# Kernel optimization log

Hardware: AMD Instinct MI355X
Metric: run time of the kernel (lower is better)

Reference implementation:

```python
import jax, jax.numpy as jnp
import numpy as np

N_NODES = 50000
N_EDGES = 800000
FEAT = 128
HID = 64
N_CLS = 12


def setup_inputs() -> dict:
    key = jax.random.key(0)
    ks = jax.random.split(key, 8)
    x = jax.random.normal(ks[0], (N_NODES, FEAT), dtype=jnp.float32)
    edge_index = jax.random.randint(ks[1], (2, N_EDGES), 0, N_NODES, dtype=jnp.int64)
    s1 = 1.0 / np.sqrt(FEAT)
    s2 = 1.0 / np.sqrt(HID)
    W1 = jax.random.uniform(ks[2], (FEAT, HID), jnp.float32, -s1, s1)
    b1 = jnp.zeros((HID,), jnp.float32)
    W2 = jax.random.uniform(ks[3], (HID, HID), jnp.float32, -s2, s2)
    b2 = jnp.zeros((HID,), jnp.float32)
    Wfc = jax.random.uniform(ks[4], (HID, N_CLS), jnp.float32, -s2, s2)
    bfc = jax.random.uniform(ks[5], (N_CLS,), jnp.float32, -s2, s2)
    return {"x": x, "edge_index": edge_index, "W1": W1, "b1": b1,
            "W2": W2, "b2": b2, "Wfc": Wfc, "bfc": bfc}


def gcn_conv(x, W, b, src, dst, n_nodes):
    """PyG GCNConv: symmetric-normalized aggregation with self-loops.
    out_i = sum_{j in N(i)} (xW)_j / sqrt(d_i d_j) + (xW)_i / d_i + b,
    where d = in-degree + 1 (self loop)."""
    xw = x @ W  # [N, out] -- transform before propagate (PyG order)
    deg = jnp.zeros((n_nodes,), x.dtype).at[dst].add(1.0) + 1.0
    dinv = jax.lax.rsqrt(deg)
    norm = dinv[src] * dinv[dst]  # [E]
    agg = jax.ops.segment_sum(xw[src] * norm[:, None], dst, num_segments=n_nodes)
    agg = agg + xw * (dinv * dinv)[:, None]  # self-loop term
    return agg + b


def reference(x, edge_index, W1, b1, W2, b2, Wfc, bfc):
    n = x.shape[0]
    src, dst = edge_index[0], edge_index[1]
    h = jax.nn.relu(gcn_conv(x, W1, b1, src, dst, n))
    h = jax.nn.relu(gcn_conv(h, W2, b2, src, dst, n))
    return h @ Wfc + bfc  # [N, num_content_categories]
```

## Files before the change

kernel.cpp:

```cpp
#include <hip/hip_runtime.h>
#include <hip/hip_fp16.h>


#define CAP   64
#define NBUK  196
#define ET    4096
#define BCAP  5120

typedef unsigned short u16;
typedef unsigned long long u64;
typedef _Float16 f16;
typedef _Float16 f16x8 __attribute__((ext_vector_type(8)));
typedef float f32x4 __attribute__((ext_vector_type(4)));

__global__ __launch_bounds__(256) void k_prep(const float* __restrict__ W1,
                                              const float* __restrict__ W2,
                                              f16* __restrict__ W1t,
                                              f16* __restrict__ W2t,
                                              int* __restrict__ gcur) {
    int i = blockIdx.x * 256 + threadIdx.x;
    if (i < NBUK) gcur[i] = 0;
    if (i < 128 * 64) {
        int k = i >> 6, nn = i & 63;
        W1t[nn * 128 + k] = (f16)W1[k * 64 + nn];
    }
    int j = i - 128 * 64;
    if (j >= 0 && j < 64 * 64) {
        int k = j >> 6, nn = j & 63;
        W2t[nn * 64 + k] = (f16)W2[k * 64 + nn];
    }
}

__global__ __launch_bounds__(256) void k_scat(const int* __restrict__ src,
                                              const int* __restrict__ dst,
                                              int* __restrict__ gcur,
                                              unsigned* __restrict__ eb, int E) {
    __shared__ int hist[NBUK];
    __shared__ int cur[NBUK];
    const int tid = threadIdx.x, blk = blockIdx.x;
    for (int i = tid; i < NBUK; i += 256) hist[i] = 0;
    __syncthreads();

    const int e0 = blk * ET;
    unsigned pk[16];
    if (e0 + ET <= E) {
        const int4* s4 = (const int4*)(src + e0);
        const int4* d4 = (const int4*)(dst + e0);
#pragma unroll
        for (int j = 0; j < ET / 1024; j++) {
            int4 sv = s4[j * 256 + tid];
            int4 dv = d4[j * 256 + tid];
            pk[4 * j + 0] = ((unsigned)dv.x << 16) | (unsigned)sv.x;
            pk[4 * j + 1] = ((unsigned)dv.y << 16) | (unsigned)sv.y;
            pk[4 * j + 2] = ((unsigned)dv.z << 16) | (unsigned)sv.z;
            pk[4 * j + 3] = ((unsigned)dv.w << 16) | (unsigned)sv.w;
            atomicAdd(&hist[(unsigned)dv.x >> 8], 1);
            atomicAdd(&hist[(unsigned)dv.y >> 8], 1);
            atomicAdd(&hist[(unsigned)dv.z >> 8], 1);
            atomicAdd(&hist[(unsigned)dv.w >> 8], 1);
        }
    } else {
#pragma unroll
        for (int j = 0; j < ET / 256; j++) {
            int e = e0 + j * 256 + tid;
            unsigned u = 0xffffffffu;
            if (e < E) {
                unsigned d = (unsigned)dst[e];
                u = (d << 16) | (unsigned)src[e];
                atomicAdd(&hist[d >> 8], 1);
            }
            pk[j] = u;
        }
    }
    __syncthreads();
    for (int b = tid; b < NBUK; b += 256)
        cur[b] = b * BCAP + atomicAdd(&gcur[b], hist[b]);
    __syncthreads();
#pragma unroll
    for (int j = 0; j < 16; j++) {
        unsigned u = pk[j];
        if (u != 0xffffffffu) eb[atomicAdd(&cur[u >> 24], 1)] = u;
    }
}

__global__ __launch_bounds__(1024) void k_buildb(const unsigned* __restrict__ eb,
                                                 const int* __restrict__ gcur,
                                                 u16* __restrict__ csr,
                                                 int* __restrict__ cnt, int n) {
    __shared__ u16 lcsr[256 * CAP];
    __shared__ int cur[256];
    const int tid = threadIdx.x, b = blockIdx.x;
    if (tid < 256) cur[tid] = 0;
    __syncthreads();
    const int e0 = b * BCAP, e1 = e0 + gcur[b];
    for (int e = e0 + tid; e < e1; e += 1024) {
        unsigned u = __builtin_nontemporal_load(eb + e);
        int ld = (int)((u >> 16) & 255u);
        int p = atomicAdd(&cur[ld], 1);
        if (p < CAP) lcsr[ld * CAP + p] = (u16)(u & 0xffffu);
    }
    __syncthreads();
    const int node0 = b * 256;
    for (int i = tid; i < 256 * CAP / 8; i += 1024) {
        int r = i / (CAP / 8), q = i % (CAP / 8);
        int c = cur[r] < CAP ? cur[r] : CAP;
        uint4 v = *(uint4*)&lcsr[r * CAP + q * 8];
        if (q * 8 >= c) v = make_uint4(0, 0, 0, 0);
        *(uint4*)&csr[(size_t)(node0 + r) * CAP + q * 8] = v;
    }
    if (tid < 256 && node0 + tid < n) cnt[node0 + tid] = cur[tid];
}

template <int K, bool IS_HALF, typename TIN>
__global__ __launch_bounds__(256) void k_gemm(const TIN* __restrict__ X,
                                              const f16* __restrict__ Wt,
                                              const int* __restrict__ cnt,
                                              __half* __restrict__ Y, int n) {
    constexpr int KS = K + 8;
    __shared__ f16 xsh[64 * KS];
    __shared__ f16 wsh[64 * KS];
    const int tid = threadIdx.x;
    const int row0 = blockIdx.x * 64;

    for (int i = tid; i < 64 * (K / 8); i += 256) {
        int nn = i / (K / 8), kq = i % (K / 8);
        *(uint4*)&wsh[nn * KS + 8 * kq] = *(const uint4*)&Wt[nn * K + 8 * kq];
    }
    if constexpr (IS_HALF) {
        const __half* Xh = (const __half*)X;
        for (int i = tid; i < 64 * (K / 8); i += 256) {
            int r = i / (K / 8), kq = i % (K / 8);
            uint4 u = make_uint4(0, 0, 0, 0);
            int row = row0 + r;
            if (row < n) u = *(const uint4*)&Xh[(size_t)row * K + 8 * kq];
            *(uint4*)&xsh[r * KS + 8 * kq] = u;
        }
    } else {
        const float* Xf = (const float*)X;
        for (int i = tid; i < 64 * (K / 4); i += 256) {
            int r = i / (K / 4), q4 = i % (K / 4);
            float4 v = make_float4(0.f, 0.f, 0.f, 0.f);
            int row = row0 + r;
            if (row < n) v = *(const float4*)&Xf[(size_t)row * K + 4 * q4];
            __half2 p0 = __floats2half2_rn(v.x, v.y);
            __half2 p1 = __floats2half2_rn(v.z, v.w);
            uint2 o = make_uint2(*(unsigned*)&p0, *(unsigned*)&p1);
            *(uint2*)&xsh[r * KS + 4 * q4] = o;
        }
    }
    __syncthreads();

    const int wv = tid >> 6;
    const int lane = tid & 63;
    const int mn = lane & 15;
    const int q = lane >> 4;

    f32x4 acc[4] = {{0, 0, 0, 0}, {0, 0, 0, 0}, {0, 0, 0, 0}, {0, 0, 0, 0}};
    const f16* arow = &xsh[(16 * wv + mn) * KS + 8 * q];
#pragma unroll
    for (int s = 0; s < K / 32; s++) {
        f16x8 A = *(const f16x8*)&arow[32 * s];
#pragma unroll
        for (int c = 0; c < 4; c++) {
            f16x8 B = *(const f16x8*)&wsh[(16 * c + mn) * KS + 32 * s + 8 * q];
            acc[c] = __builtin_amdgcn_mfma_f32_16x16x32_f16(A, B, acc[c], 0, 0, 0);
        }
    }

    const int rowb = row0 + 16 * wv + 4 * q;
    float dinv[4];
#pragma unroll
    for (int r = 0; r < 4; r++)
        dinv[r] = rsqrtf((float)((rowb + r < n) ? cnt[rowb + r] : 0) + 1.0f);
#pragma unroll
    for (int c = 0; c < 4; c++)
#pragma unroll
        for (int r = 0; r < 4; r++) {
            int row = rowb + r;
            if (row < n)
                Y[(size_t)row * 64 + 16 * c + mn] = __float2half(acc[c][r] * dinv[r]);
        }
}

__device__ __forceinline__ float4 gather_node(const __half* __restrict__ y,
                                              const u16* __restrict__ lst,
                                              int deg, int c4) {
    float4 a0 = make_float4(0.f, 0.f, 0.f, 0.f);
    float4 a1 = make_float4(0.f, 0.f, 0.f, 0.f);
    int i = 0;
    for (; i + 16 <= deg; i += 16) {
        const u64* lp = (const u64*)(lst + i);
        u64 q0 = __builtin_nontemporal_load(lp);
        u64 q1 = __builtin_nontemporal_load(lp + 1);
        u64 q2 = __builtin_nontemporal_load(lp + 2);
        u64 q3 = __builtin_nontemporal_load(lp + 3);
        unsigned idx[16];
#pragma unroll
        for (int t = 0; t < 4; t++) {
            idx[t]      = (unsigned)((q0 >> (16 * t)) & 0xffffu);
            idx[t + 4]  = (unsigned)((q1 >> (16 * t)) & 0xffffu);
            idx[t + 8]  = (unsigned)((q2 >> (16 * t)) & 0xffffu);
            idx[t + 12] = (unsigned)((q3 >> (16 * t)) & 0xffffu);
        }
        uint2 v[16];
#pragma unroll
        for (int t = 0; t < 16; t++) v[t] = *(const uint2*)&y[(size_t)idx[t] * 64 + 4 * c4];
#pragma unroll
        for (int t = 0; t < 16; t += 2) {
            float2 lo0 = __half22float2(*(__half2*)&v[t].x);
            float2 hi0 = __half22float2(*(__half2*)&v[t].y);
            float2 lo1 = __half22float2(*(__half2*)&v[t + 1].x);
            float2 hi1 = __half22float2(*(__half2*)&v[t + 1].y);
            a0.x += lo0.x; a0.y += lo0.y; a0.z += hi0.x; a0.w += hi0.y;
            a1.x += lo1.x; a1.y += lo1.y; a1.z += hi1.x; a1.w += hi1.y;
        }
    }
    if (i + 8 <= deg) {
        const u64* lp = (const u64*)(lst + i);
        u64 q0 = __builtin_nontemporal_load(lp);
        u64 q1 = __builtin_nontemporal_load(lp + 1);
        unsigned idx[8];
#pragma unroll
        for (int t = 0; t < 4; t++) {
            idx[t]     = (unsigned)((q0 >> (16 * t)) & 0xffffu);
            idx[t + 4] = (unsigned)((q1 >> (16 * t)) & 0xffffu);
        }
        uint2 v[8];
#pragma unroll
        for (int t = 0; t < 8; t++) v[t] = *(const uint2*)&y[(size_t)idx[t] * 64 + 4 * c4];
#pragma unroll
        for (int t = 0; t < 8; t += 2) {
            float2 lo0 = __half22float2(*(__half2*)&v[t].x);
            float2 hi0 = __half22float2(*(__half2*)&v[t].y);
            float2 lo1 = __half22float2(*(__half2*)&v[t + 1].x);
            float2 hi1 = __half22float2(*(__half2*)&v[t + 1].y);
            a0.x += lo0.x; a0.y += lo0.y; a0.z += hi0.x; a0.w += hi0.y;
            a1.x += lo1.x; a1.y += lo1.y; a1.z += hi1.x; a1.w += hi1.y;
        }
        i += 8;
    }
    if (i + 4 <= deg) {
        u64 q0 = __builtin_nontemporal_load((const u64*)(lst + i));
        unsigned idx[4];
#pragma unroll
        for (int t = 0; t < 4; t++) idx[t] = (unsigned)((q0 >> (16 * t)) & 0xffffu);
        uint2 v[4];
#pragma unroll
        for (int t = 0; t < 4; t++) v[t] = *(const uint2*)&y[(size_t)idx[t] * 64 + 4 * c4];
#pragma unroll
        for (int t = 0; t < 4; t += 2) {
            float2 lo0 = __half22float2(*(__half2*)&v[t].x);
            float2 hi0 = __half22float2(*(__half2*)&v[t].y);
            float2 lo1 = __half22float2(*(__half2*)&v[t + 1].x);
            float2 hi1 = __half22float2(*(__half2*)&v[t + 1].y);
            a0.x += lo0.x; a0.y += lo0.y; a0.z += hi0.x; a0.w += hi0.y;
            a1.x += lo1.x; a1.y += lo1.y; a1.z += hi1.x; a1.w += hi1.y;
        }
        i += 4;
    }
    for (; i < deg; i++) {
        uint2 vv = *(const uint2*)&y[(size_t)lst[i] * 64 + 4 * c4];
        float2 lo = __half22float2(*(__half2*)&vv.x);
        float2 hi = __half22float2(*(__half2*)&vv.y);
        a0.x += lo.x; a0.y += lo.y; a0.z += hi.x; a0.w += hi.y;
    }
    return make_float4(a0.x + a1.x, a0.y + a1.y, a0.z + a1.z, a0.w + a1.w);
}

__global__ __launch_bounds__(256) void k_agg1g2(const __half* __restrict__ y,
                                                const u16* __restrict__ csr,
                                                const int* __restrict__ cnt,
                                                const float* __restrict__ bias,
                                                const f16* __restrict__ W2t,
                                                __half* __restrict__ y2, int n) {
    constexpr int KS2 = 64 + 8;
    __shared__ f16 ash[16 * KS2];
    __shared__ f16 wsh[64 * KS2];
    __shared__ float dsh[16];
    const int tid = threadIdx.x;
    const int node0 = blockIdx.x * 16;

    for (int i = tid; i < 64 * 8; i += 256) {
        int nn = i >> 3, kq = i & 7;
        *(uint4*)&wsh[nn * KS2 + 8 * kq] = *(const uint4*)&W2t[nn * 64 + 8 * kq];
    }

    const int c4 = tid & 15;
    const int r16 = tid >> 4;
    const int node = node0 + r16;
    const int nodeC = node < n ? node : 0;
    int deg_raw = (node < n) ? cnt[node] : 0;
    int deg = deg_raw > CAP ? CAP : deg_raw;
    float4 acc = gather_node(y, csr + (size_t)nodeC * CAP, deg, c4);
    uint2 sv = *(const uint2*)&y[(size_t)nodeC * 64 + 4 * c4];
    float2 slo = __half22float2(*(__half2*)&sv.x);
    float2 shi = __half22float2(*(__half2*)&sv.y);
    float d = rsqrtf((float)deg_raw + 1.0f);
    float4 bv = *(const float4*)&bias[4 * c4];
    float v0 = fmaxf(fmaf(d, acc.x + slo.x, bv.x), 0.f);
    float v1 = fmaxf(fmaf(d, acc.y + slo.y, bv.y), 0.f);
    float v2 = fmaxf(fmaf(d, acc.z + shi.x, bv.z), 0.f);
    float v3 = fmaxf(fmaf(d, acc.w + shi.y, bv.w), 0.f);
    __half2 o0 = __floats2half2_rn(v0, v1);
    __half2 o1 = __floats2half2_rn(v2, v3);
    u64 packed = (u64)(*(unsigned*)&o0) | ((u64)(*(unsigned*)&o1) << 32);
    *(u64*)&ash[r16 * KS2 + 4 * c4] = packed;
    if (c4 == 0) dsh[r16] = d;
    __syncthreads();

    const int wv = tid >> 6;
    const int lane = tid & 63;
    const int mn = lane & 15;
    const int q = lane >> 4;
    f32x4 acc2 = {0, 0, 0, 0};
#pragma unroll
    for (int s = 0; s < 2; s++) {
        f16x8 A = *(const f16x8*)&ash[mn * KS2 + 32 * s + 8 * q];
        f16x8 B = *(const f16x8*)&wsh[(16 * wv + mn) * KS2 + 32 * s + 8 * q];
        acc2 = __builtin_amdgcn_mfma_f32_16x16x32_f16(A, B, acc2, 0, 0, 0);
    }
#pragma unroll
    for (int r = 0; r < 4; r++) {
        int row = node0 + 4 * q + r;
        if (row < n)
            y2[(size_t)row * 64 + 16 * wv + mn] =
                __float2half(acc2[r] * dsh[4 * q + r]);
    }
}

__global__ __launch_bounds__(256) void k_agg2fc(const __half* __restrict__ y,
                                                const u16* __restrict__ csr,
                                                const int* __restrict__ cnt,
                                                const float* __restrict__ bias,
                                                const float* __restrict__ Wfc,
                                                const float* __restrict__ bfc,
                                                float* __restrict__ out, int n) {
    __shared__ float wf[12 * 64];
    __shared__ float bf[12];
    const int tid = threadIdx.x;
    for (int i = tid; i < 12 * 64; i += 256) {
        int c = i >> 6, k = i & 63;
        wf[i] = Wfc[k * 12 + c];
    }
    if (tid < 12) bf[tid] = bfc[tid];
    __syncthreads();

    const int c4 = tid & 15;
    const int node = blockIdx.x * 16 + (tid >> 4);
    if (node >= n) return;
    int deg_raw = cnt[node];
    int deg = deg_raw > CAP ? CAP : deg_raw;
    float4 acc = gather_node(y, csr + node * CAP, deg, c4);
    uint2 sv = *(const uint2*)&y[(size_t)node * 64 + 4 * c4];
    float2 slo = __half22float2(*(__half2*)&sv.x);
    float2 shi = __half22float2(*(__half2*)&sv.y);
    float d = rsqrtf((float)deg_raw + 1.0f);
    float4 bv = *(const float4*)&bias[4 * c4];
    float v0 = fmaxf(fmaf(d, acc.x + slo.x, bv.x), 0.f);
    float v1 = fmaxf(fmaf(d, acc.y + slo.y, bv.y), 0.f);
    float v2 = fmaxf(fmaf(d, acc.z + shi.x, bv.z), 0.f);
    float v3 = fmaxf(fmaf(d, acc.w + shi.y, bv.w), 0.f);

    float res = 0.f;
#pragma unroll
    for (int c = 0; c < 12; c++) {
        float4 wv = *(const float4*)&wf[c * 64 + 4 * c4];
        float p = v0 * wv.x + v1 * wv.y + v2 * wv.z + v3 * wv.w;
        p += __shfl_xor(p, 1);
        p += __shfl_xor(p, 2);
        p += __shfl_xor(p, 4);
        p += __shfl_xor(p, 8);
        if (c4 == c) res = p + bf[c];
    }
    if (c4 < 12) out[(size_t)node * 12 + c4] = res;
}

extern "C" void kernel_launch(void* const* d_in, const int* in_sizes, int n_in,
                              void* d_out, int out_size, void* d_ws, size_t ws_size,
                              hipStream_t stream) {
    const float* x   = (const float*)d_in[0];
    const int*   ei  = (const int*)d_in[1];
    const float* W1  = (const float*)d_in[2];
    const float* b1  = (const float*)d_in[3];
    const float* W2  = (const float*)d_in[4];
    const float* b2  = (const float*)d_in[5];
    const float* Wfc = (const float*)d_in[6];
    const float* bfc = (const float*)d_in[7];
    float* out = (float*)d_out;

    const int n = in_sizes[0] / 128;
    const int E = in_sizes[1] / 2;
    const int* src = ei;
    const int* dst = ei + E;
    const int nblk = (E + ET - 1) / ET;

    char* w = (char*)d_ws;
    unsigned* eb  = (unsigned*)w;  w += (size_t)NBUK * BCAP * 4;
    int* gcur     = (int*)w;       w += 256 * 4;
    int* cnt      = (int*)w;       w += (size_t)((n + 63) / 64) * 64 * 4;
    f16* W1t      = (f16*)w;       w += 128 * 64 * 2;
    f16* W2t      = (f16*)w;       w += 64 * 64 * 2 + 256;
    u16* csr      = (u16*)w;       w += (size_t)NBUK * 256 * CAP * 2;
    __half* y     = (__half*)w;    w += (size_t)n * 64 * 2;
    __half* y2    = (__half*)w;

    k_prep   <<<dim3(48), dim3(256), 0, stream>>>(W1, W2, W1t, W2t, gcur);
    k_scat   <<<dim3(nblk), dim3(256), 0, stream>>>(src, dst, gcur, eb, E);
    k_buildb <<<dim3(NBUK), dim3(1024), 0, stream>>>(eb, gcur, csr, cnt, n);
    k_gemm<128, false, float><<<dim3((n + 63) / 64), dim3(256), 0, stream>>>(x, W1t, cnt, y, n);
    k_agg1g2 <<<dim3((n + 15) / 16), dim3(256), 0, stream>>>(y, csr, cnt, b1, W2t, y2, n);
    k_agg2fc <<<dim3((n + 15) / 16), dim3(256), 0, stream>>>(y2, csr, cnt, b2, Wfc, bfc, out, n);
}
```

Before: 156.7 us.

## Split neighbor lists by source half and gather in two passes per persistent block

The CSR build now keeps each node's neighbours in two 32-slot halves, split by whether the source index is below n/2, and packs both counts into one int. The aggregation kernels become persistent blocks (grid 1024) that first gather the low-half neighbours for all their node groups into shared memory, then gather the high-half and finish. Each pass then touches only half of the feature table, which is meant to improve L2/cache locality of the random gathers. The cost is more passes, a lower per-half cap (degree over 32 in one half gets truncated), extra shared memory, and a fixed NG_MAX=4 that assumes ngroups ≤ 4096.

Result: slower. 188.5 us (+20.3%).

```diff
diff --git a/kernel.cpp b/kernel.cpp
--- a/kernel.cpp
+++ b/kernel.cpp
@@ -3,9 +3,12 @@
 
 
 #define CAP   64
+#define HCAP  32
 #define NBUK  196
 #define ET    4096
 #define BCAP  5120
+#define AGG_GRID 1024
+#define NG_MAX 4
 
 typedef unsigned short u16;
 typedef unsigned long long u64;
@@ -86,37 +89,42 @@
 __global__ __launch_bounds__(1024) void k_buildb(const unsigned* __restrict__ eb,
                                                  const int* __restrict__ gcur,
                                                  u16* __restrict__ csr,
-                                                 int* __restrict__ cnt, int n) {
+                                                 int* __restrict__ cnt,
+                                                 int n, int hthr) {
     __shared__ u16 lcsr[256 * CAP];
-    __shared__ int cur[256];
+    __shared__ int cur[512];
     const int tid = threadIdx.x, b = blockIdx.x;
-    if (tid < 256) cur[tid] = 0;
+    if (tid < 512) cur[tid] = 0;
     __syncthreads();
     const int e0 = b * BCAP, e1 = e0 + gcur[b];
     for (int e = e0 + tid; e < e1; e += 1024) {
         unsigned u = __builtin_nontemporal_load(eb + e);
         int ld = (int)((u >> 16) & 255u);
-        int p = atomicAdd(&cur[ld], 1);
-        if (p < CAP) lcsr[ld * CAP + p] = (u16)(u & 0xffffu);
+        int srcv = (int)(u & 0xffffu);
+        int hf = srcv >= hthr;
+        int p = atomicAdd(&cur[ld * 2 + hf], 1);
+        if (p < HCAP) lcsr[ld * CAP + hf * HCAP + p] = (u16)srcv;
     }
     __syncthreads();
     const int node0 = b * 256;
     for (int i = tid; i < 256 * CAP / 8; i += 1024) {
-        int r = i / (CAP / 8), q = i % (CAP / 8);
-        int c = cur[r] < CAP ? cur[r] : CAP;
+        int r = i >> 3, q = i & 7;
+        int hf = q >= (HCAP / 8);
+        int cc = cur[r * 2 + hf]; if (cc > HCAP) cc = HCAP;
+        int off = q * 8 - hf * HCAP;
         uint4 v = *(uint4*)&lcsr[r * CAP + q * 8];
-        if (q * 8 >= c) v = make_uint4(0, 0, 0, 0);
+        if (off >= cc) v = make_uint4(0, 0, 0, 0);
         *(uint4*)&csr[(size_t)(node0 + r) * CAP + q * 8] = v;
     }
-    if (tid < 256 && node0 + tid < n) cnt[node0 + tid] = cur[tid];
-}
-
-template <int K, bool IS_HALF, typename TIN>
-__global__ __launch_bounds__(256) void k_gemm(const TIN* __restrict__ X,
-                                              const f16* __restrict__ Wt,
-                                              const int* __restrict__ cnt,
-                                              __half* __restrict__ Y, int n) {
-    constexpr int KS = K + 8;
+    if (tid < 256 && node0 + tid < n)
+        cnt[node0 + tid] = cur[tid * 2] | (cur[tid * 2 + 1] << 16);
+}
+
+__global__ __launch_bounds__(256) void k_gemm1(const float* __restrict__ X,
+                                               const f16* __restrict__ Wt,
+                                               const int* __restrict__ cnt,
+                                               __half* __restrict__ Y, int n) {
+    constexpr int K = 128, KS = K + 8;
     __shared__ f16 xsh[64 * KS];
     __shared__ f16 wsh[64 * KS];
     const int tid = threadIdx.x;
@@ -126,27 +134,15 @@
         int nn = i / (K / 8), kq = i % (K / 8);
         *(uint4*)&wsh[nn * KS + 8 * kq] = *(const uint4*)&Wt[nn * K + 8 * kq];
     }
-    if constexpr (IS_HALF) {
-        const __half* Xh = (const __half*)X;
-        for (int i = tid; i < 64 * (K / 8); i += 256) {
-            int r = i / (K / 8), kq = i % (K / 8);
-            uint4 u = make_uint4(0, 0, 0, 0);
-            int row = row0 + r;
-            if (row < n) u = *(const uint4*)&Xh[(size_t)row * K + 8 * kq];
-            *(uint4*)&xsh[r * KS + 8 * kq] = u;
-        }
-    } else {
-        const float* Xf = (const float*)X;
-        for (int i = tid; i < 64 * (K / 4); i += 256) {
-            int r = i / (K / 4), q4 = i % (K / 4);
-            float4 v = make_float4(0.f, 0.f, 0.f, 0.f);
-            int row = row0 + r;
-            if (row < n) v = *(const float4*)&Xf[(size_t)row * K + 4 * q4];
-            __half2 p0 = __floats2half2_rn(v.x, v.y);
-            __half2 p1 = __floats2half2_rn(v.z, v.w);
-            uint2 o = make_uint2(*(unsigned*)&p0, *(unsigned*)&p1);
-            *(uint2*)&xsh[r * KS + 4 * q4] = o;
-        }
+    for (int i = tid; i < 64 * (K / 4); i += 256) {
+        int r = i / (K / 4), q4 = i % (K / 4);
+        float4 v = make_float4(0.f, 0.f, 0.f, 0.f);
+        int row = row0 + r;
+        if (row < n) v = *(const float4*)&X[(size_t)row * K + 4 * q4];
+        __half2 p0 = __floats2half2_rn(v.x, v.y);
+        __half2 p1 = __floats2half2_rn(v.z, v.w);
+        uint2 o = make_uint2(*(unsigned*)&p0, *(unsigned*)&p1);
+        *(uint2*)&xsh[r * KS + 4 * q4] = o;
     }
     __syncthreads();
 
@@ -170,8 +166,10 @@
     const int rowb = row0 + 16 * wv + 4 * q;
     float dinv[4];
 #pragma unroll
-    for (int r = 0; r < 4; r++)
-        dinv[r] = rsqrtf((float)((rowb + r < n) ? cnt[rowb + r] : 0) + 1.0f);
+    for (int r = 0; r < 4; r++) {
+        int cp = (rowb + r < n) ? cnt[rowb + r] : 0;
+        dinv[r] = rsqrtf((float)((cp & 0xffff) + (cp >> 16)) + 1.0f);
+    }
 #pragma unroll
     for (int c = 0; c < 4; c++)
 #pragma unroll
@@ -267,18 +265,20 @@
     return make_float4(a0.x + a1.x, a0.y + a1.y, a0.z + a1.z, a0.w + a1.w);
 }
 
-__global__ __launch_bounds__(256) void k_agg1g2(const __half* __restrict__ y,
-                                                const u16* __restrict__ csr,
-                                                const int* __restrict__ cnt,
-                                                const float* __restrict__ bias,
-                                                const f16* __restrict__ W2t,
-                                                __half* __restrict__ y2, int n) {
+__global__ __launch_bounds__(256, 4) void k_agg1g2(const __half* __restrict__ y,
+                                                   const u16* __restrict__ csr,
+                                                   const int* __restrict__ cnt,
+                                                   const float* __restrict__ bias,
+                                                   const f16* __restrict__ W2t,
+                                                   __half* __restrict__ y2, int n) {
     constexpr int KS2 = 64 + 8;
     __shared__ f16 ash[16 * KS2];
     __shared__ f16 wsh[64 * KS2];
     __shared__ float dsh[16];
+    __shared__ float4 pash[NG_MAX][256];
     const int tid = threadIdx.x;
-    const int node0 = blockIdx.x * 16;
+    const int G = gridDim.x;
+    const int ngroups = (n + 15) >> 4;
 
     for (int i = tid; i < 64 * 8; i += 256) {
         int nn = i >> 3, kq = i & 7;
@@ -287,57 +287,78 @@
 
     const int c4 = tid & 15;
     const int r16 = tid >> 4;
-    const int node = node0 + r16;
-    const int nodeC = node < n ? node : 0;
-    int deg_raw = (node < n) ? cnt[node] : 0;
-    int deg = deg_raw > CAP ? CAP : deg_raw;
-    float4 acc = gather_node(y, csr + (size_t)nodeC * CAP, deg, c4);
-    uint2 sv = *(const uint2*)&y[(size_t)nodeC * 64 + 4 * c4];
-    float2 slo = __half22float2(*(__half2*)&sv.x);
-    float2 shi = __half22float2(*(__half2*)&sv.y);
-    float d = rsqrtf((float)deg_raw + 1.0f);
-    float4 bv = *(const float4*)&bias[4 * c4];
-    float v0 = fmaxf(fmaf(d, acc.x + slo.x, bv.x), 0.f);
-    float v1 = fmaxf(fmaf(d, acc.y + slo.y, bv.y), 0.f);
-    float v2 = fmaxf(fmaf(d, acc.z + shi.x, bv.z), 0.f);
-    float v3 = fmaxf(fmaf(d, acc.w + shi.y, bv.w), 0.f);
-    __half2 o0 = __floats2half2_rn(v0, v1);
-    __half2 o1 = __floats2half2_rn(v2, v3);
-    u64 packed = (u64)(*(unsigned*)&o0) | ((u64)(*(unsigned*)&o1) << 32);
-    *(u64*)&ash[r16 * KS2 + 4 * c4] = packed;
-    if (c4 == 0) dsh[r16] = d;
-    __syncthreads();
-
-    const int wv = tid >> 6;
-    const int lane = tid & 63;
-    const int mn = lane & 15;
-    const int q = lane >> 4;
-    f32x4 acc2 = {0, 0, 0, 0};
-#pragma unroll
-    for (int s = 0; s < 2; s++) {
-        f16x8 A = *(const f16x8*)&ash[mn * KS2 + 32 * s + 8 * q];
-        f16x8 B = *(const f16x8*)&wsh[(16 * wv + mn) * KS2 + 32 * s + 8 * q];
-        acc2 = __builtin_amdgcn_mfma_f32_16x16x32_f16(A, B, acc2, 0, 0, 0);
-    }
-#pragma unroll
-    for (int r = 0; r < 4; r++) {
-        int row = node0 + 4 * q + r;
-        if (row < n)
-            y2[(size_t)row * 64 + 16 * wv + mn] =
-                __float2half(acc2[r] * dsh[4 * q + r]);
-    }
-}
-
-__global__ __launch_bounds__(256) void k_agg2fc(const __half* __restrict__ y,
-                                                const u16* __restrict__ csr,
-                                                const int* __restrict__ cnt,
-                                                const float* __restrict__ bias,
-                                                const float* __restrict__ Wfc,
-                                                const float* __restrict__ bfc,
-                                                float* __restrict__ out, int n) {
+
+    int gi = 0;
+    for (int g = blockIdx.x; g < ngroups; g += G, ++gi) {
+        const int node = g * 16 + r16;
+        const int nodeC = node < n ? node : 0;
+        int cp = (node < n) ? cnt[node] : 0;
+        int dlo = cp & 0xffff; if (dlo > HCAP) dlo = HCAP;
+        pash[gi][tid] = gather_node(y, csr + (size_t)nodeC * CAP, dlo, c4);
+    }
+
+    gi = 0;
+    for (int g = blockIdx.x; g < ngroups; g += G, ++gi) {
+        const int node0g = g * 16;
+        const int node = node0g + r16;
+        const int nodeC = node < n ? node : 0;
+        int cp = (node < n) ? cnt[node] : 0;
+        int dlo_raw = cp & 0xffff, dhi_raw = cp >> 16;
+        int dhi = dhi_raw > HCAP ? HCAP : dhi_raw;
+        float4 acc = gather_node(y, csr + (size_t)nodeC * CAP + HCAP, dhi, c4);
+        float4 pa = pash[gi][tid];
+        acc.x += pa.x; acc.y += pa.y; acc.z += pa.z; acc.w += pa.w;
+        uint2 sv = *(const uint2*)&y[(size_t)nodeC * 64 + 4 * c4];
+        float2 slo = __half22float2(*(__half2*)&sv.x);
+        float2 shi = __half22float2(*(__half2*)&sv.y);
+        float d = rsqrtf((float)(dlo_raw + dhi_raw) + 1.0f);
+        float4 bv = *(const float4*)&bias[4 * c4];
+        float v0 = fmaxf(fmaf(d, acc.x + slo.x, bv.x), 0.f);
+        float v1 = fmaxf(fmaf(d, acc.y + slo.y, bv.y), 0.f);
+        float v2 = fmaxf(fmaf(d, acc.z + shi.x, bv.z), 0.f);
+        float v3 = fmaxf(fmaf(d, acc.w + shi.y, bv.w), 0.f);
+        __half2 o0 = __floats2half2_rn(v0, v1);
+        __half2 o1 = __floats2half2_rn(v2, v3);
+        u64 packed = (u64)(*(unsigned*)&o0) | ((u64)(*(unsigned*)&o1) << 32);
+        *(u64*)&ash[r16 * KS2 + 4 * c4] = packed;
+        if (c4 == 0) dsh[r16] = d;
+        __syncthreads();
+
+        const int wv = tid >> 6;
+        const int lane = tid & 63;
+        const int mn = lane & 15;
+        const int q = lane >> 4;
+        f32x4 acc2 = {0, 0, 0, 0};
+#pragma unroll
+        for (int s = 0; s < 2; s++) {
+            f16x8 A = *(const f16x8*)&ash[mn * KS2 + 32 * s + 8 * q];
+            f16x8 B = *(const f16x8*)&wsh[(16 * wv + mn) * KS2 + 32 * s + 8 * q];
+            acc2 = __builtin_amdgcn_mfma_f32_16x16x32_f16(A, B, acc2, 0, 0, 0);
+        }
+#pragma unroll
+        for (int r = 0; r < 4; r++) {
+            int row = node0g + 4 * q + r;
+            if (row < n)
+                y2[(size_t)row * 64 + 16 * wv + mn] =
+                    __float2half(acc2[r] * dsh[4 * q + r]);
+        }
+        __syncthreads();
+    }
+}
+
+__global__ __launch_bounds__(256, 4) void k_agg2fc(const __half* __restrict__ y,
+                                                   const u16* __restrict__ csr,
+                                                   const int* __restrict__ cnt,
+                                                   const float* __restrict__ bias,
+                                                   const float* __restrict__ Wfc,
+                                                   const float* __restrict__ bfc,
+                                                   float* __restrict__ out, int n) {
     __shared__ float wf[12 * 64];
     __shared__ float bf[12];
+    __shared__ float4 pash[NG_MAX][256];
     const int tid = threadIdx.x;
+    const int G = gridDim.x;
+    const int ngroups = (n + 15) >> 4;
     for (int i = tid; i < 12 * 64; i += 256) {
         int c = i >> 6, k = i & 63;
         wf[i] = Wfc[k * 12 + c];
@@ -346,33 +367,50 @@
     __syncthreads();
 
     const int c4 = tid & 15;
-    const int node = blockIdx.x * 16 + (tid >> 4);
-    if (node >= n) return;
-    int deg_raw = cnt[node];
-    int deg = deg_raw > CAP ? CAP : deg_raw;
-    float4 acc = gather_node(y, csr + node * CAP, deg, c4);
-    uint2 sv = *(const uint2*)&y[(size_t)node * 64 + 4 * c4];
-    float2 slo = __half22float2(*(__half2*)&sv.x);
-    float2 shi = __half22float2(*(__half2*)&sv.y);
-    float d = rsqrtf((float)deg_raw + 1.0f);
-    float4 bv = *(const float4*)&bias[4 * c4];
-    float v0 = fmaxf(fmaf(d, acc.x + slo.x, bv.x), 0.f);
-    float v1 = fmaxf(fmaf(d, acc.y + slo.y, bv.y), 0.f);
-    float v2 = fmaxf(fmaf(d, acc.z + shi.x, bv.z), 0.f);
-    float v3 = fmaxf(fmaf(d, acc.w + shi.y, bv.w), 0.f);
-
-    float res = 0.f;
-#pragma unroll
-    for (int c = 0; c < 12; c++) {
-        float4 wv = *(const float4*)&wf[c * 64 + 4 * c4];
-        float p = v0 * wv.x + v1 * wv.y + v2 * wv.z + v3 * wv.w;
-        p += __shfl_xor(p, 1);
-        p += __shfl_xor(p, 2);
-        p += __shfl_xor(p, 4);
-        p += __shfl_xor(p, 8);
-        if (c4 == c) res = p + bf[c];
-    }
-    if (c4 < 12) out[(size_t)node * 12 + c4] = res;
+    const int r16 = tid >> 4;
+
+    int gi = 0;
+    for (int g = blockIdx.x; g < ngroups; g += G, ++gi) {
+        const int node = g * 16 + r16;
+        const int nodeC = node < n ? node : 0;
+        int cp = (node < n) ? cnt[node] : 0;
+        int dlo = cp & 0xffff; if (dlo > HCAP) dlo = HCAP;
+        pash[gi][tid] = gather_node(y, csr + (size_t)nodeC * CAP, dlo, c4);
+    }
+
+    gi = 0;
+    for (int g = blockIdx.x; g < ngroups; g += G, ++gi) {
+        const int node = g * 16 + r16;
+        const int nodeC = node < n ? node : 0;
+        int cp = (node < n) ? cnt[node] : 0;
+        int dlo_raw = cp & 0xffff, dhi_raw = cp >> 16;
+        int dhi = dhi_raw > HCAP ? HCAP : dhi_raw;
+        float4 acc = gather_node(y, csr + (size_t)nodeC * CAP + HCAP, dhi, c4);
+        float4 pa = pash[gi][tid];
+        acc.x += pa.x; acc.y += pa.y; acc.z += pa.z; acc.w += pa.w;
+        uint2 sv = *(const uint2*)&y[(size_t)nodeC * 64 + 4 * c4];
+        float2 slo = __half22float2(*(__half2*)&sv.x);
+        float2 shi = __half22float2(*(__half2*)&sv.y);
+        float d = rsqrtf((float)(dlo_raw + dhi_raw) + 1.0f);
+        float4 bv = *(const float4*)&bias[4 * c4];
+        float v0 = fmaxf(fmaf(d, acc.x + slo.x, bv.x), 0.f);
+        float v1 = fmaxf(fmaf(d, acc.y + slo.y, bv.y), 0.f);
+        float v2 = fmaxf(fmaf(d, acc.z + shi.x, bv.z), 0.f);
+        float v3 = fmaxf(fmaf(d, acc.w + shi.y, bv.w), 0.f);
+
+        float res = 0.f;
+#pragma unroll
+        for (int c = 0; c < 12; c++) {
+            float4 wv = *(const float4*)&wf[c * 64 + 4 * c4];
+            float p = v0 * wv.x + v1 * wv.y + v2 * wv.z + v3 * wv.w;
+            p += __shfl_xor(p, 1);
+            p += __shfl_xor(p, 2);
+            p += __shfl_xor(p, 4);
+            p += __shfl_xor(p, 8);
+            if (c4 == c) res = p + bf[c];
+        }
+        if (c4 < 12 && node < n) out[(size_t)node * 12 + c4] = res;
+    }
 }
 
 extern "C" void kernel_launch(void* const* d_in, const int* in_sizes, int n_in,
@@ -406,8 +444,8 @@
 
     k_prep   <<<dim3(48), dim3(256), 0, stream>>>(W1, W2, W1t, W2t, gcur);
     k_scat   <<<dim3(nblk), dim3(256), 0, stream>>>(src, dst, gcur, eb, E);
-    k_buildb <<<dim3(NBUK), dim3(1024), 0, stream>>>(eb, gcur, csr, cnt, n);
-    k_gemm<128, false, float><<<dim3((n + 63) / 64), dim3(256), 0, stream>>>(x, W1t, cnt, y, n);
-    k_agg1g2 <<<dim3((n + 15) / 16), dim3(256), 0, stream>>>(y, csr, cnt, b1, W2t, y2, n);
-    k_agg2fc <<<dim3((n + 15) / 16), dim3(256), 0, stream>>>(y2, csr, cnt, b2, Wfc, bfc, out, n);
-}
+    k_buildb <<<dim3(NBUK), dim3(1024), 0, stream>>>(eb, gcur, csr, cnt, n, n / 2);
+    k_gemm1  <<<dim3((n + 63) / 64), dim3(256), 0, stream>>>(x, W1t, cnt, y, n);
+    k_agg1g2 <<<dim3(AGG_GRID), dim3(256), 0, stream>>>(y, csr, cnt, b1, W2t, y2, n);
+    k_agg2fc <<<dim3(AGG_GRID), dim3(256), 0, stream>>>(y2, csr, cnt, b2, Wfc, bfc, out, n);
+}
```

## Merge edge scatter and first GEMM into one launch, defer degree scaling

Applied to the files above, without the earlier changes.

The edge bucketing kernel and the layer-1 X*W1 GEMM now run as disjoint block ranges of a single launch, so the GEMM no longer waits for the degree count. The GEMM writes an unscaled fp32 intermediate, and the CSR build kernel then applies the rsqrt degree scaling and converts to fp16. This removes one kernel launch and its dependency bubble. In exchange it adds an extra fp32 write and read of an N x 64 buffer and more LDS per block in the merged kernel, which may reduce occupancy for the scatter blocks.

Result: no change. 156.4 us (-0.2%).

```diff
diff --git a/kernel.cpp b/kernel.cpp
--- a/kernel.cpp
+++ b/kernel.cpp
@@ -31,62 +31,119 @@
     }
 }
 
-__global__ __launch_bounds__(256) void k_scat(const int* __restrict__ src,
-                                              const int* __restrict__ dst,
-                                              int* __restrict__ gcur,
-                                              unsigned* __restrict__ eb, int E) {
+__global__ __launch_bounds__(256) void k_scatgemm(const int* __restrict__ src,
+                                                  const int* __restrict__ dst,
+                                                  int* __restrict__ gcur,
+                                                  unsigned* __restrict__ eb, int E,
+                                                  const float* __restrict__ X,
+                                                  const f16* __restrict__ W1t,
+                                                  float* __restrict__ Z,
+                                                  int n, int nblk) {
+    constexpr int K = 128, KS = K + 8;
+    __shared__ f16 xsh[64 * KS];
+    __shared__ f16 wsh[64 * KS];
     __shared__ int hist[NBUK];
     __shared__ int cur[NBUK];
-    const int tid = threadIdx.x, blk = blockIdx.x;
-    for (int i = tid; i < NBUK; i += 256) hist[i] = 0;
-    __syncthreads();
-
-    const int e0 = blk * ET;
-    unsigned pk[16];
-    if (e0 + ET <= E) {
-        const int4* s4 = (const int4*)(src + e0);
-        const int4* d4 = (const int4*)(dst + e0);
-#pragma unroll
-        for (int j = 0; j < ET / 1024; j++) {
-            int4 sv = s4[j * 256 + tid];
-            int4 dv = d4[j * 256 + tid];
-            pk[4 * j + 0] = ((unsigned)dv.x << 16) | (unsigned)sv.x;
-            pk[4 * j + 1] = ((unsigned)dv.y << 16) | (unsigned)sv.y;
-            pk[4 * j + 2] = ((unsigned)dv.z << 16) | (unsigned)sv.z;
-            pk[4 * j + 3] = ((unsigned)dv.w << 16) | (unsigned)sv.w;
-            atomicAdd(&hist[(unsigned)dv.x >> 8], 1);
-            atomicAdd(&hist[(unsigned)dv.y >> 8], 1);
-            atomicAdd(&hist[(unsigned)dv.z >> 8], 1);
-            atomicAdd(&hist[(unsigned)dv.w >> 8], 1);
+    const int tid = threadIdx.x;
+
+    if (blockIdx.x < (unsigned)nblk) {
+        const int blk = blockIdx.x;
+        for (int i = tid; i < NBUK; i += 256) hist[i] = 0;
+        __syncthreads();
+
+        const int e0 = blk * ET;
+        unsigned pk[16];
+        if (e0 + ET <= E) {
+            const int4* s4 = (const int4*)(src + e0);
+            const int4* d4 = (const int4*)(dst + e0);
+#pragma unroll
+            for (int j = 0; j < ET / 1024; j++) {
+                int4 sv = s4[j * 256 + tid];
+                int4 dv = d4[j * 256 + tid];
+                pk[4 * j + 0] = ((unsigned)dv.x << 16) | (unsigned)sv.x;
+                pk[4 * j + 1] = ((unsigned)dv.y << 16) | (unsigned)sv.y;
+                pk[4 * j + 2] = ((unsigned)dv.z << 16) | (unsigned)sv.z;
+                pk[4 * j + 3] = ((unsigned)dv.w << 16) | (unsigned)sv.w;
+                atomicAdd(&hist[(unsigned)dv.x >> 8], 1);
+                atomicAdd(&hist[(unsigned)dv.y >> 8], 1);
+                atomicAdd(&hist[(unsigned)dv.z >> 8], 1);
+                atomicAdd(&hist[(unsigned)dv.w >> 8], 1);
+            }
+        } else {
+#pragma unroll
+            for (int j = 0; j < ET / 256; j++) {
+                int e = e0 + j * 256 + tid;
+                unsigned u = 0xffffffffu;
+                if (e < E) {
+                    unsigned d = (unsigned)dst[e];
+                    u = (d << 16) | (unsigned)src[e];
+                    atomicAdd(&hist[d >> 8], 1);
+                }
+                pk[j] = u;
+            }
+        }
+        __syncthreads();
+        for (int b = tid; b < NBUK; b += 256)
+            cur[b] = b * BCAP + atomicAdd(&gcur[b], hist[b]);
+        __syncthreads();
+#pragma unroll
+        for (int j = 0; j < 16; j++) {
+            unsigned u = pk[j];
+            if (u != 0xffffffffu) eb[atomicAdd(&cur[u >> 24], 1)] = u;
         }
     } else {
-#pragma unroll
-        for (int j = 0; j < ET / 256; j++) {
-            int e = e0 + j * 256 + tid;
-            unsigned u = 0xffffffffu;
-            if (e < E) {
-                unsigned d = (unsigned)dst[e];
-                u = (d << 16) | (unsigned)src[e];
-                atomicAdd(&hist[d >> 8], 1);
+        const int row0 = (blockIdx.x - nblk) * 64;
+
+        for (int i = tid; i < 64 * (K / 8); i += 256) {
+            int nn = i / (K / 8), kq = i % (K / 8);
+            *(uint4*)&wsh[nn * KS + 8 * kq] = *(const uint4*)&W1t[nn * K + 8 * kq];
+        }
+        for (int i = tid; i < 64 * (K / 4); i += 256) {
+            int r = i / (K / 4), q4 = i % (K / 4);
+            float4 v = make_float4(0.f, 0.f, 0.f, 0.f);
+            int row = row0 + r;
+            if (row < n) v = *(const float4*)&X[(size_t)row * K + 4 * q4];
+            __half2 p0 = __floats2half2_rn(v.x, v.y);
+            __half2 p1 = __floats2half2_rn(v.z, v.w);
+            uint2 o = make_uint2(*(unsigned*)&p0, *(unsigned*)&p1);
+            *(uint2*)&xsh[r * KS + 4 * q4] = o;
+        }
+        __syncthreads();
+
+        const int wv = tid >> 6;
+        const int lane = tid & 63;
+        const int mn = lane & 15;
+        const int q = lane >> 4;
+
+        f32x4 acc[4] = {{0, 0, 0, 0}, {0, 0, 0, 0}, {0, 0, 0, 0}, {0, 0, 0, 0}};
+        const f16* arow = &xsh[(16 * wv + mn) * KS + 8 * q];
+#pragma unroll
+        for (int s = 0; s < K / 32; s++) {
+            f16x8 A = *(const f16x8*)&arow[32 * s];
+#pragma unroll
+            for (int c = 0; c < 4; c++) {
+                f16x8 B = *(const f16x8*)&wsh[(16 * c + mn) * KS + 32 * s + 8 * q];
+                acc[c] = __builtin_amdgcn_mfma_f32_16x16x32_f16(A, B, acc[c], 0, 0, 0);
             }
-            pk[j] = u;
-        }
-    }
-    __syncthreads();
-    for (int b = tid; b < NBUK; b += 256)
-        cur[b] = b * BCAP + atomicAdd(&gcur[b], hist[b]);
-    __syncthreads();
-#pragma unroll
-    for (int j = 0; j < 16; j++) {
-        unsigned u = pk[j];
-        if (u != 0xffffffffu) eb[atomicAdd(&cur[u >> 24], 1)] = u;
+        }
+
+        const int rowb = row0 + 16 * wv + 4 * q;
+#pragma unroll
+        for (int c = 0; c < 4; c++)
+#pragma unroll
+            for (int r = 0; r < 4; r++) {
+                int row = rowb + r;
+                if (row < n) Z[(size_t)row * 64 + 16 * c + mn] = acc[c][r];
+            }
     }
 }
 
 __global__ __launch_bounds__(1024) void k_buildb(const unsigned* __restrict__ eb,
                                                  const int* __restrict__ gcur,
                                                  u16* __restrict__ csr,
-                                                 int* __restrict__ cnt, int n) {
+                                                 int* __restrict__ cnt,
+                                                 const float* __restrict__ z,
+                                                 __half* __restrict__ y, int n) {
     __shared__ u16 lcsr[256 * CAP];
     __shared__ int cur[256];
     const int tid = threadIdx.x, b = blockIdx.x;
@@ -109,77 +166,18 @@
         *(uint4*)&csr[(size_t)(node0 + r) * CAP + q * 8] = v;
     }
     if (tid < 256 && node0 + tid < n) cnt[node0 + tid] = cur[tid];
-}
-
-template <int K, bool IS_HALF, typename TIN>
-__global__ __launch_bounds__(256) void k_gemm(const TIN* __restrict__ X,
-                                              const f16* __restrict__ Wt,
-                                              const int* __restrict__ cnt,
-                                              __half* __restrict__ Y, int n) {
-    constexpr int KS = K + 8;
-    __shared__ f16 xsh[64 * KS];
-    __shared__ f16 wsh[64 * KS];
-    const int tid = threadIdx.x;
-    const int row0 = blockIdx.x * 64;
-
-    for (int i = tid; i < 64 * (K / 8); i += 256) {
-        int nn = i / (K / 8), kq = i % (K / 8);
-        *(uint4*)&wsh[nn * KS + 8 * kq] = *(const uint4*)&Wt[nn * K + 8 * kq];
-    }
-    if constexpr (IS_HALF) {
-        const __half* Xh = (const __half*)X;
-        for (int i = tid; i < 64 * (K / 8); i += 256) {
-            int r = i / (K / 8), kq = i % (K / 8);
-            uint4 u = make_uint4(0, 0, 0, 0);
-            int row = row0 + r;
-            if (row < n) u = *(const uint4*)&Xh[(size_t)row * K + 8 * kq];
-            *(uint4*)&xsh[r * KS + 8 * kq] = u;
-        }
-    } else {
-        const float* Xf = (const float*)X;
-        for (int i = tid; i < 64 * (K / 4); i += 256) {
-            int r = i / (K / 4), q4 = i % (K / 4);
-            float4 v = make_float4(0.f, 0.f, 0.f, 0.f);
-            int row = row0 + r;
-            if (row < n) v = *(const float4*)&Xf[(size_t)row * K + 4 * q4];
-            __half2 p0 = __floats2half2_rn(v.x, v.y);
-            __half2 p1 = __floats2half2_rn(v.z, v.w);
-            uint2 o = make_uint2(*(unsigned*)&p0, *(unsigned*)&p1);
-            *(uint2*)&xsh[r * KS + 4 * q4] = o;
-        }
-    }
-    __syncthreads();
-
-    const int wv = tid >> 6;
-    const int lane = tid & 63;
-    const int mn = lane & 15;
-    const int q = lane >> 4;
-
-    f32x4 acc[4] = {{0, 0, 0, 0}, {0, 0, 0, 0}, {0, 0, 0, 0}, {0, 0, 0, 0}};
-    const f16* arow = &xsh[(16 * wv + mn) * KS + 8 * q];
-#pragma unroll
-    for (int s = 0; s < K / 32; s++) {
-        f16x8 A = *(const f16x8*)&arow[32 * s];
-#pragma unroll
-        for (int c = 0; c < 4; c++) {
-            f16x8 B = *(const f16x8*)&wsh[(16 * c + mn) * KS + 32 * s + 8 * q];
-            acc[c] = __builtin_amdgcn_mfma_f32_16x16x32_f16(A, B, acc[c], 0, 0, 0);
-        }
-    }
-
-    const int rowb = row0 + 16 * wv + 4 * q;
-    float dinv[4];
-#pragma unroll
-    for (int r = 0; r < 4; r++)
-        dinv[r] = rsqrtf((float)((rowb + r < n) ? cnt[rowb + r] : 0) + 1.0f);
-#pragma unroll
-    for (int c = 0; c < 4; c++)
-#pragma unroll
-        for (int r = 0; r < 4; r++) {
-            int row = rowb + r;
-            if (row < n)
-                Y[(size_t)row * 64 + 16 * c + mn] = __float2half(acc[c][r] * dinv[r]);
-        }
+    for (int i = tid; i < 256 * 16; i += 1024) {
+        int r = i >> 4, q = i & 15;
+        int node = node0 + r;
+        if (node < n) {
+            float d = rsqrtf((float)cur[r] + 1.0f);
+            float4 v = *(const float4*)&z[(size_t)node * 64 + 4 * q];
+            __half2 p0 = __floats2half2_rn(v.x * d, v.y * d);
+            __half2 p1 = __floats2half2_rn(v.z * d, v.w * d);
+            *(uint2*)&y[(size_t)node * 64 + 4 * q] =
+                make_uint2(*(unsigned*)&p0, *(unsigned*)&p1);
+        }
+    }
 }
 
 __device__ __forceinline__ float4 gather_node(const __half* __restrict__ y,
@@ -393,6 +391,7 @@
     const int* src = ei;
     const int* dst = ei + E;
     const int nblk = (E + ET - 1) / ET;
+    const int ntile = (n + 63) / 64;
 
     char* w = (char*)d_ws;
     unsigned* eb  = (unsigned*)w;  w += (size_t)NBUK * BCAP * 4;
@@ -401,13 +400,14 @@
     f16* W1t      = (f16*)w;       w += 128 * 64 * 2;
     f16* W2t      = (f16*)w;       w += 64 * 64 * 2 + 256;
     u16* csr      = (u16*)w;       w += (size_t)NBUK * 256 * CAP * 2;
+    float* z      = (float*)w;     w += (size_t)((n + 63) / 64) * 64 * 64 * 4;
     __half* y     = (__half*)w;    w += (size_t)n * 64 * 2;
     __half* y2    = (__half*)w;
 
-    k_prep   <<<dim3(48), dim3(256), 0, stream>>>(W1, W2, W1t, W2t, gcur);
-    k_scat   <<<dim3(nblk), dim3(256), 0, stream>>>(src, dst, gcur, eb, E);
-    k_buildb <<<dim3(NBUK), dim3(1024), 0, stream>>>(eb, gcur, csr, cnt, n);
-    k_gemm<128, false, float><<<dim3((n + 63) / 64), dim3(256), 0, stream>>>(x, W1t, cnt, y, n);
-    k_agg1g2 <<<dim3((n + 15) / 16), dim3(256), 0, stream>>>(y, csr, cnt, b1, W2t, y2, n);
-    k_agg2fc <<<dim3((n + 15) / 16), dim3(256), 0, stream>>>(y2, csr, cnt, b2, Wfc, bfc, out, n);
-}
+    k_prep    <<<dim3(48), dim3(256), 0, stream>>>(W1, W2, W1t, W2t, gcur);
+    k_scatgemm<<<dim3(nblk + ntile), dim3(256), 0, stream>>>(src, dst, gcur, eb, E,
+                                                             x, W1t, z, n, nblk);
+    k_buildb  <<<dim3(NBUK), dim3(1024), 0, stream>>>(eb, gcur, csr, cnt, z, y, n);
+    k_agg1g2  <<<dim3((n + 15) / 16), dim3(256), 0, stream>>>(y, csr, cnt, b1, W2t, y2, n);
+    k_agg2fc  <<<dim3((n + 15) / 16), dim3(256), 0, stream>>>(y2, csr, cnt, b2, Wfc, bfc, out, n);
+}
```
